# Optimization experiments

Hardware: AMD Instinct MI355X
Metric: run time of the kernel (lower is better)

## Reference

```python
import jax, jax.numpy as jnp
import numpy as np

DIM = 768
NUM_HEADS = 12
HEAD_DIM = DIM // NUM_HEADS
SCALE = HEAD_DIM ** -0.5


def setup_inputs() -> dict:
    key = jax.random.key(0)
    ks = jax.random.split(key, 6)
    B, N, C = 4, 2048, DIM
    x = jax.random.normal(ks[0], (B, N, C), dtype=jnp.float32)
    qkv_weight = jax.random.normal(ks[1], (3 * C, C), dtype=jnp.float32) * (C ** -0.5)
    q_bias = jax.random.normal(ks[2], (C,), dtype=jnp.float32) * 0.02
    v_bias = jax.random.normal(ks[3], (C,), dtype=jnp.float32) * 0.02
    proj_weight = jax.random.normal(ks[4], (C, C), dtype=jnp.float32) * (C ** -0.5)
    proj_bias = jax.random.normal(ks[5], (C,), dtype=jnp.float32) * 0.02
    return {"x": x, "qkv_weight": qkv_weight, "q_bias": q_bias,
            "v_bias": v_bias, "proj_weight": proj_weight, "proj_bias": proj_bias}


def reference(x, qkv_weight, q_bias, v_bias, proj_weight, proj_bias):
    B, N, C = x.shape
    # bias = concat(q_bias, zeros_like(v_bias), v_bias)
    bias = jnp.concatenate([q_bias, jnp.zeros_like(v_bias), v_bias])
    qkv = x @ qkv_weight.T + bias                      # [B, N, 3C]
    qkv = qkv.reshape(B, N, 3, NUM_HEADS, HEAD_DIM)
    q, k, v = jnp.moveaxis(qkv, 2, 0)                  # each [B, N, H, hd]
    q = jnp.transpose(q, (0, 2, 1, 3)) * SCALE         # [B, H, N, hd]
    k = jnp.transpose(k, (0, 2, 1, 3))
    v = jnp.transpose(v, (0, 2, 1, 3))
    attn = jax.nn.softmax(jnp.einsum('bhqd,bhkd->bhqk', q, k), axis=-1)
    out = jnp.einsum('bhqk,bhkd->bhqd', attn, v)       # [B, H, N, hd]
    out = jnp.transpose(out, (0, 2, 1, 3)).reshape(B, N, C)
    return out @ proj_weight.T + proj_bias
```

## Files before the change

kernel.cpp:

```cpp
#include <hip/hip_runtime.h>
#include <cstdint>
#include <cstddef>

typedef _Float16 f16;
typedef _Float16 f16x8 __attribute__((ext_vector_type(8)));
typedef _Float16 f16x4 __attribute__((ext_vector_type(4)));
typedef __fp16 h16x2 __attribute__((ext_vector_type(2)));
typedef float f32x4 __attribute__((ext_vector_type(4)));

#define DIM 768
#define NHEAD 12
#define HD 64
#define BATCH 4
#define SEQ 2048
#define MROWS (BATCH*SEQ)
#define C3 (3*DIM)
#define NBH (BATCH*NHEAD)

__device__ __forceinline__ f32x4 mfma32(f16x8 a, f16x8 b, f32x4 c) {
  return __builtin_amdgcn_mfma_f32_16x16x32_f16(a, b, c, 0, 0, 0);
}
__device__ __forceinline__ f32x4 mfma16(f16x4 a, f16x4 b, f32x4 c) {
  return __builtin_amdgcn_mfma_f32_16x16x16f16(a, b, c, 0, 0, 0);
}

__device__ __forceinline__ void gl2lds16(const void* g, void* l) {
  __builtin_amdgcn_global_load_lds(
      (const __attribute__((address_space(1))) void*)g,
      (__attribute__((address_space(3))) void*)l, 16, 0, 0);
}

__global__ __launch_bounds__(256) void k_convert(
    const float* __restrict__ x, const float* __restrict__ wqkv,
    const float* __restrict__ wproj,
    f16* __restrict__ xh, f16* __restrict__ wqh, f16* __restrict__ wph)
{
  const int NX = MROWS*DIM/4, NW = C3*DIM/4;
  int i = blockIdx.x * 256 + threadIdx.x;
  const float4* src; f16* dst; int idx;
  if (i < NX)         { src = (const float4*)x;     dst = xh;  idx = i; }
  else if (i < NX+NW) { src = (const float4*)wqkv;  dst = wqh; idx = i - NX; }
  else                { src = (const float4*)wproj; dst = wph; idx = i - NX - NW; }
  float4 v = src[idx];
  union { f16 h[4]; uint64_t u; } r;
  r.h[0] = (f16)v.x; r.h[1] = (f16)v.y; r.h[2] = (f16)v.z; r.h[3] = (f16)v.w;
  ((uint64_t*)dst)[idx] = r.u;
}

__device__ __forceinline__ void gemm_tile(
    const f16* __restrict__ A, const f16* __restrict__ B,
    int lda, int ldb, int K, int m0, int n0,
    f16* sA, f16* sB, f32x4 acc[4][4])
{
  const int tid = threadIdx.x, wid = tid >> 6;
  const int lane = tid & 63, lane15 = lane & 15, quad = lane >> 4;
  const int wm = wid >> 1, wn = wid & 1;
  for (int k0 = 0; k0 < K; k0 += 64) {
    __syncthreads();
    #pragma unroll
    for (int i = 0; i < 4; i++) {
      int j = i*256 + tid;
      int row = j >> 3;
      int sc  = (j & 7) ^ (row & 7);
      gl2lds16(A + (size_t)(m0 + row)*lda + k0 + sc*8, sA + (i*256 + wid*64)*8);
      gl2lds16(B + (size_t)(n0 + row)*ldb + k0 + sc*8, sB + (i*256 + wid*64)*8);
    }
    __syncthreads();
    #pragma unroll
    for (int ks = 0; ks < 2; ks++) {
      f16x8 af[4], bf[4];
      #pragma unroll
      for (int t = 0; t < 4; t++) {
        int ra = wm*64 + t*16 + lane15;
        af[t] = *(const f16x8*)(sA + ra*64 + (((ks*4 + quad) ^ (ra & 7)) << 3));
        int rb = wn*64 + t*16 + lane15;
        bf[t] = *(const f16x8*)(sB + rb*64 + (((ks*4 + quad) ^ (rb & 7)) << 3));
      }
      #pragma unroll
      for (int mt = 0; mt < 4; mt++)
        #pragma unroll
        for (int nt = 0; nt < 4; nt++)
          acc[mt][nt] = mfma32(af[mt], bf[nt], acc[mt][nt]);
    }
  }
}

__global__ __launch_bounds__(256, 2) void k_qkv(
    const f16* __restrict__ xh, const f16* __restrict__ wqh,
    const float* __restrict__ q_bias, const float* __restrict__ v_bias,
    f16* __restrict__ Qh, f16* __restrict__ Kh, f16* __restrict__ Vt)
{
  __shared__ f16 sA[128*64], sB[128*64];
  __shared__ f16 sT[128*136];
  f32x4 acc[4][4];
  const f32x4 z4 = {0.f, 0.f, 0.f, 0.f};
  #pragma unroll
  for (int a = 0; a < 4; a++)
    #pragma unroll
    for (int b = 0; b < 4; b++) acc[a][b] = z4;

  const int m0 = blockIdx.y * 128, n0 = blockIdx.x * 128;
  gemm_tile(xh, wqh, DIM, DIM, DIM, m0, n0, sA, sB, acc);

  const int tid = threadIdx.x, wid = tid >> 6, lane = tid & 63;
  const int lane15 = lane & 15, quad = lane >> 4;
  const int wm = wid >> 1, wn = wid & 1;
  const int bb = m0 >> 11, nbase = m0 & (SEQ - 1);
  const float QS = 0.125f * 1.4426950408889634f;

  if (n0 < 2*DIM) {
    const bool isQ = (n0 < DIM);
    #pragma unroll
    for (int nt = 0; nt < 4; nt++) {
      int col_l = wn*64 + nt*16 + lane15;
      int col = n0 + col_l;
      float b = isQ ? q_bias[col] : 0.f;
      #pragma unroll
      for (int mt = 0; mt < 4; mt++)
        #pragma unroll
        for (int r = 0; r < 4; r++) {
          int m_l = wm*64 + mt*16 + quad*4 + r;
          float v = acc[mt][nt][r] + b;
          if (isQ) v *= QS;
          sT[m_l*136 + col_l] = (f16)v;
        }
    }
    __syncthreads();
    #pragma unroll
    for (int it = 0; it < 8; it++) {
      int idx = it*256 + tid;
      int m_l = idx >> 4, ch = idx & 15;
      f16x8 val = *(const f16x8*)(sT + m_l*136 + ch*8);
      int col = n0 + ch*8;
      int c2 = isQ ? col : (col - DIM);
      int h = c2 >> 6, d = c2 & 63;
      f16* dst = isQ ? Qh : Kh;
      *(f16x8*)(dst + (((size_t)(bb*NHEAD + h)*SEQ + nbase + m_l) << 6) + d) = val;
    }
  } else {
    #pragma unroll
    for (int nt = 0; nt < 4; nt++) {
      int col_l = wn*64 + nt*16 + lane15;
      int c2 = n0 - 2*DIM + col_l;
      float b = v_bias[c2];
      #pragma unroll
      for (int mt = 0; mt < 4; mt++)
        #pragma unroll
        for (int r = 0; r < 4; r++) {
          int m_l = wm*64 + mt*16 + quad*4 + r;
          sT[col_l*136 + m_l] = (f16)(acc[mt][nt][r] + b);
        }
    }
    __syncthreads();
    #pragma unroll
    for (int it = 0; it < 8; it++) {
      int idx = it*256 + tid;
      int d_l = idx >> 4, m8 = idx & 15;
      f16x8 val = *(const f16x8*)(sT + d_l*136 + m8*8);
      int c2 = n0 - 2*DIM + d_l;
      int h = c2 >> 6, d = c2 & 63;
      *(f16x8*)(Vt + ((size_t)(bb*NHEAD + h)*HD + d)*SEQ + nbase + m8*8) = val;
    }
  }
}

#define KVT 128
__global__ __launch_bounds__(256, 3) void k_attn(
    const f16* __restrict__ Qh, const f16* __restrict__ Kh,
    const f16* __restrict__ Vt, f16* __restrict__ attnh)
{
  __shared__ f16 smem[4*32*72];
  f16* sV = smem;

  const int tid = threadIdx.x, wid = tid >> 6, lane = tid & 63;
  const int lane15 = lane & 15, quad = lane >> 4;
  const int q0 = blockIdx.x * 128;
  const int bh = blockIdx.y;
  const int qw = q0 + wid*32;

  f16x8 qf[2][2];
  #pragma unroll
  for (int qt = 0; qt < 2; qt++)
    #pragma unroll
    for (int ks = 0; ks < 2; ks++)
      qf[qt][ks] = *(const f16x8*)(Qh + ((size_t)bh*SEQ + qw + qt*16 + lane15)*HD
                                      + ks*32 + quad*8);

  f32x4 o[4][2];
  f32x4 sacc[2];
  const f32x4 z4 = {0.f, 0.f, 0.f, 0.f};
  #pragma unroll
  for (int dt = 0; dt < 4; dt++)
    #pragma unroll
    for (int qt = 0; qt < 2; qt++) o[dt][qt] = z4;
  sacc[0] = z4; sacc[1] = z4;
  const f16x4 one4 = {(f16)1.f, (f16)1.f, (f16)1.f, (f16)1.f};

  const f16* Kbh = Kh + (size_t)bh*SEQ*HD;

  for (int kv0 = 0; kv0 < SEQ; kv0 += KVT) {
    __syncthreads();
    #pragma unroll
    for (int i = 0; i < 4; i++) {
      int j = i*256 + tid;
      int row = j >> 4;
      int sc  = (j & 15) ^ (row & 7);
      gl2lds16(Vt + ((size_t)bh*HD + row)*SEQ + kv0 + sc*8, sV + (i*256 + wid*64)*8);
    }
    __syncthreads();
    const f16* Kt = Kbh + (size_t)kv0*HD;

    #pragma unroll
    for (int c = 0; c < 4; c++) {
      f16x8 ka[2][2];
      #pragma unroll
      for (int kt = 0; kt < 2; kt++)
        #pragma unroll
        for (int ks = 0; ks < 2; ks++)
          ka[ks][kt] = *(const f16x8*)(Kt + (size_t)(c*32 + kt*16 + lane15)*HD
                                          + ks*32 + quad*8);
      f32x4 s[2][2];
      #pragma unroll
      for (int kt = 0; kt < 2; kt++)
        #pragma unroll
        for (int qt = 0; qt < 2; qt++) s[kt][qt] = z4;
      #pragma unroll
      for (int ks = 0; ks < 2; ks++)
        #pragma unroll
        for (int kt = 0; kt < 2; kt++)
          #pragma unroll
          for (int qt = 0; qt < 2; qt++)
            s[kt][qt] = mfma32(ka[ks][kt], qf[qt][ks], s[kt][qt]);

      f16x4 pb[2][2];
      #pragma unroll
      for (int kt = 0; kt < 2; kt++)
        #pragma unroll
        for (int qt = 0; qt < 2; qt++) {
          union { h16x2 g2[2]; f16x4 h4; } u;
          u.g2[0] = __builtin_amdgcn_cvt_pkrtz(exp2f(s[kt][qt][0]), exp2f(s[kt][qt][1]));
          u.g2[1] = __builtin_amdgcn_cvt_pkrtz(exp2f(s[kt][qt][2]), exp2f(s[kt][qt][3]));
          pb[kt][qt] = u.h4;
        }
      #pragma unroll
      for (int kt = 0; kt < 2; kt++)
        #pragma unroll
        for (int qt = 0; qt < 2; qt++)
          sacc[qt] = mfma16(one4, pb[kt][qt], sacc[qt]);

      #pragma unroll
      for (int dt = 0; dt < 4; dt++) {
        int row = dt*16 + lane15;
        #pragma unroll
        for (int kt = 0; kt < 2; kt++) {
          int c16 = 4*c + 2*kt + (quad >> 1);
          const f16* vp = sV + row*KVT + (((c16 ^ (row & 7)) << 3)) + (quad & 1)*4;
          f16x4 va = *(const f16x4*)vp;
          #pragma unroll
          for (int qt = 0; qt < 2; qt++)
            o[dt][qt] = mfma16(va, pb[kt][qt], o[dt][qt]);
        }
      }
    }
  }

  float inv[2] = {1.f / sacc[0][0], 1.f / sacc[1][0]};

  __syncthreads();
  f16* tb = smem + wid * (32 * 72);
  #pragma unroll
  for (int dt = 0; dt < 4; dt++)
    #pragma unroll
    for (int qt = 0; qt < 2; qt++) {
      f32x4 v = o[dt][qt];
      float iv = inv[qt];
      f16x4 hx = {(f16)(v[0]*iv), (f16)(v[1]*iv), (f16)(v[2]*iv), (f16)(v[3]*iv)};
      *(f16x4*)(tb + (qt*16 + lane15)*72 + dt*16 + quad*4) = hx;
    }
  const int b = bh / NHEAD, h = bh % NHEAD;
  #pragma unroll
  for (int i = 0; i < 4; i++) {
    int row = i*8 + (lane >> 3);
    f16x8 rv = *(const f16x8*)(tb + row*72 + (lane & 7)*8);
    *(f16x8*)(attnh + ((size_t)b*SEQ + qw + row)*DIM + h*HD + (lane & 7)*8) = rv;
  }
}

__global__ __launch_bounds__(256, 2) void k_proj(
    const f16* __restrict__ ah, const f16* __restrict__ wph,
    const float* __restrict__ pbias, float* __restrict__ out)
{
  __shared__ f16 sA[128*64], sB[128*64];
  f32x4 acc[4][4];
  const f32x4 z4 = {0.f, 0.f, 0.f, 0.f};
  #pragma unroll
  for (int a = 0; a < 4; a++)
    #pragma unroll
    for (int b = 0; b < 4; b++) acc[a][b] = z4;

  const int m0 = blockIdx.y * 128, n0 = blockIdx.x * 128;
  gemm_tile(ah, wph, DIM, DIM, DIM, m0, n0, sA, sB, acc);

  const int tid = threadIdx.x, wid = tid >> 6, lane = tid & 63;
  const int lane15 = lane & 15, quad = lane >> 4;
  const int wm = wid >> 1, wn = wid & 1;
  #pragma unroll
  for (int nt = 0; nt < 4; nt++) {
    int col = n0 + wn*64 + nt*16 + lane15;
    float bias = pbias[col];
    #pragma unroll
    for (int mt = 0; mt < 4; mt++) {
      #pragma unroll
      for (int r = 0; r < 4; r++) {
        int m = m0 + wm*64 + mt*16 + quad*4 + r;
        out[(size_t)m*DIM + col] = acc[mt][nt][r] + bias;
      }
    }
  }
}

extern "C" void kernel_launch(void* const* d_in, const int* in_sizes, int n_in,
                              void* d_out, int out_size, void* d_ws, size_t ws_size,
                              hipStream_t stream) {
  const float* x    = (const float*)d_in[0];
  const float* wqkv = (const float*)d_in[1];
  const float* qb   = (const float*)d_in[2];
  const float* vb   = (const float*)d_in[3];
  const float* wp   = (const float*)d_in[4];
  const float* pb   = (const float*)d_in[5];
  float* out = (float*)d_out;

  f16* p = (f16*)d_ws;
  f16* xh  = p; p += (size_t)MROWS*DIM;
  f16* wqh = p; p += (size_t)C3*DIM;
  f16* wph = p; p += (size_t)DIM*DIM;
  f16* Qh  = p; p += (size_t)NBH*SEQ*HD;
  f16* Kh  = p; p += (size_t)NBH*SEQ*HD;
  f16* Vt  = p; p += (size_t)NBH*SEQ*HD;
  f16* attnh = xh;

  k_convert<<<8448, 256, 0, stream>>>(x, wqkv, wp, xh, wqh, wph);
  k_qkv<<<dim3(C3/128, MROWS/128), 256, 0, stream>>>(xh, wqh, qb, vb, Qh, Kh, Vt);
  k_attn<<<dim3(SEQ/128, NBH), 256, 0, stream>>>(Qh, Kh, Vt, attnh);
  k_proj<<<dim3(DIM/128, MROWS/128), 256, 0, stream>>>(attnh, wph, pb, out);
}
```

Measured before the change: 254.9 us.

## Double-buffer GEMM tiles and stage K/V through LDS with prefetch in attention

```diff
diff --git a/kernel.cpp b/kernel.cpp
--- a/kernel.cpp
+++ b/kernel.cpp
@@ -50,13 +50,15 @@
 __device__ __forceinline__ void gemm_tile(
     const f16* __restrict__ A, const f16* __restrict__ B,
     int lda, int ldb, int K, int m0, int n0,
-    f16* sA, f16* sB, f32x4 acc[4][4])
-{
+    f16* smem, f32x4 acc[4][4])
+{
+  f16* sA0 = smem;          f16* sA1 = smem + 8192;
+  f16* sB0 = smem + 16384;  f16* sB1 = smem + 24576;
   const int tid = threadIdx.x, wid = tid >> 6;
   const int lane = tid & 63, lane15 = lane & 15, quad = lane >> 4;
   const int wm = wid >> 1, wn = wid & 1;
-  for (int k0 = 0; k0 < K; k0 += 64) {
-    __syncthreads();
+
+  auto stage = [&](int k0, f16* sA, f16* sB) {
     #pragma unroll
     for (int i = 0; i < 4; i++) {
       int j = i*256 + tid;
@@ -65,16 +67,25 @@
       gl2lds16(A + (size_t)(m0 + row)*lda + k0 + sc*8, sA + (i*256 + wid*64)*8);
       gl2lds16(B + (size_t)(n0 + row)*ldb + k0 + sc*8, sB + (i*256 + wid*64)*8);
     }
-    __syncthreads();
+  };
+
+  const int NK = K >> 6;
+  stage(0, sA0, sB0);
+  for (int kk = 0; kk < NK; kk++) {
+    f16* cA = (kk & 1) ? sA1 : sA0;
+    f16* cB = (kk & 1) ? sB1 : sB0;
+    __syncthreads();
+    if (kk + 1 < NK)
+      stage((kk + 1) << 6, (kk & 1) ? sA0 : sA1, (kk & 1) ? sB0 : sB1);
     #pragma unroll
     for (int ks = 0; ks < 2; ks++) {
       f16x8 af[4], bf[4];
       #pragma unroll
       for (int t = 0; t < 4; t++) {
         int ra = wm*64 + t*16 + lane15;
-        af[t] = *(const f16x8*)(sA + ra*64 + (((ks*4 + quad) ^ (ra & 7)) << 3));
+        af[t] = *(const f16x8*)(cA + ra*64 + (((ks*4 + quad) ^ (ra & 7)) << 3));
         int rb = wn*64 + t*16 + lane15;
-        bf[t] = *(const f16x8*)(sB + rb*64 + (((ks*4 + quad) ^ (rb & 7)) << 3));
+        bf[t] = *(const f16x8*)(cB + rb*64 + (((ks*4 + quad) ^ (rb & 7)) << 3));
       }
       #pragma unroll
       for (int mt = 0; mt < 4; mt++)
@@ -90,8 +101,7 @@
     const float* __restrict__ q_bias, const float* __restrict__ v_bias,
     f16* __restrict__ Qh, f16* __restrict__ Kh, f16* __restrict__ Vt)
 {
-  __shared__ f16 sA[128*64], sB[128*64];
-  __shared__ f16 sT[128*136];
+  __shared__ f16 smem[32768];
   f32x4 acc[4][4];
   const f32x4 z4 = {0.f, 0.f, 0.f, 0.f};
   #pragma unroll
@@ -100,13 +110,16 @@
     for (int b = 0; b < 4; b++) acc[a][b] = z4;
 
   const int m0 = blockIdx.y * 128, n0 = blockIdx.x * 128;
-  gemm_tile(xh, wqh, DIM, DIM, DIM, m0, n0, sA, sB, acc);
+  gemm_tile(xh, wqh, DIM, DIM, DIM, m0, n0, smem, acc);
 
   const int tid = threadIdx.x, wid = tid >> 6, lane = tid & 63;
   const int lane15 = lane & 15, quad = lane >> 4;
   const int wm = wid >> 1, wn = wid & 1;
   const int bb = m0 >> 11, nbase = m0 & (SEQ - 1);
   const float QS = 0.125f * 1.4426950408889634f;
+
+  f16* sT = smem;
+  __syncthreads();
 
   if (n0 < 2*DIM) {
     const bool isQ = (n0 < DIM);
@@ -165,12 +178,15 @@
 }
 
 #define KVT 128
+#define NIT (SEQ/KVT)
 __global__ __launch_bounds__(256, 3) void k_attn(
     const f16* __restrict__ Qh, const f16* __restrict__ Kh,
     const f16* __restrict__ Vt, f16* __restrict__ attnh)
 {
-  __shared__ f16 smem[4*32*72];
-  f16* sV = smem;
+  __shared__ f16 smem[2*8192 + 64*132];
+  f16* sK0 = smem;
+  f16* sK1 = smem + 8192;
+  f16* sV  = smem + 16384;
 
   const int tid = threadIdx.x, wid = tid >> 6, lane = tid & 63;
   const int lane15 = lane & 15, quad = lane >> 4;
@@ -178,6 +194,9 @@
   const int bh = blockIdx.y;
   const int qw = q0 + wid*32;
 
+  const f16* Kbh = Kh + (size_t)bh*SEQ*HD;
+  const f16* Vbh = Vt + (size_t)bh*HD*SEQ;
+
   f16x8 qf[2][2];
   #pragma unroll
   for (int qt = 0; qt < 2; qt++)
@@ -196,29 +215,51 @@
   sacc[0] = z4; sacc[1] = z4;
   const f16x4 one4 = {(f16)1.f, (f16)1.f, (f16)1.f, (f16)1.f};
 
-  const f16* Kbh = Kh + (size_t)bh*SEQ*HD;
-
-  for (int kv0 = 0; kv0 < SEQ; kv0 += KVT) {
-    __syncthreads();
+  const int vrow = tid >> 2, vcg = (tid & 3) * 32;
+  const f16* vsrc = Vbh + (size_t)vrow*SEQ + vcg;
+
+  auto stageK = [&](int kv0, f16* sK) {
     #pragma unroll
     for (int i = 0; i < 4; i++) {
       int j = i*256 + tid;
-      int row = j >> 4;
-      int sc  = (j & 15) ^ (row & 7);
-      gl2lds16(Vt + ((size_t)bh*HD + row)*SEQ + kv0 + sc*8, sV + (i*256 + wid*64)*8);
-    }
-    __syncthreads();
-    const f16* Kt = Kbh + (size_t)kv0*HD;
+      int row = j >> 3;
+      int sc  = (j & 7) ^ (row & 7);
+      gl2lds16(Kbh + (size_t)(kv0 + row)*HD + sc*8, sK + (i*256 + wid*64)*8);
+    }
+  };
+
+  stageK(0, sK0);
+  f16x8 vreg[4];
+  #pragma unroll
+  for (int j = 0; j < 4; j++) vreg[j] = *(const f16x8*)(vsrc + j*8);
+
+  for (int it = 0; it < NIT; it++) {
+    f16* cK = (it & 1) ? sK1 : sK0;
+    __syncthreads();
+    #pragma unroll
+    for (int j = 0; j < 4; j++) {
+      union { f16x8 v; f16x4 h[2]; } u; u.v = vreg[j];
+      *(f16x4*)(sV + vrow*132 + vcg + j*8)     = u.h[0];
+      *(f16x4*)(sV + vrow*132 + vcg + j*8 + 4) = u.h[1];
+    }
+    __syncthreads();
+    if (it + 1 < NIT) {
+      stageK((it + 1)*KVT, (it & 1) ? sK0 : sK1);
+      #pragma unroll
+      for (int j = 0; j < 4; j++)
+        vreg[j] = *(const f16x8*)(vsrc + (it + 1)*KVT + j*8);
+    }
 
     #pragma unroll
     for (int c = 0; c < 4; c++) {
       f16x8 ka[2][2];
       #pragma unroll
-      for (int kt = 0; kt < 2; kt++)
+      for (int kt = 0; kt < 2; kt++) {
+        int rb = c*32 + kt*16 + lane15;
         #pragma unroll
         for (int ks = 0; ks < 2; ks++)
-          ka[ks][kt] = *(const f16x8*)(Kt + (size_t)(c*32 + kt*16 + lane15)*HD
-                                          + ks*32 + quad*8);
+          ka[ks][kt] = *(const f16x8*)(cK + rb*64 + (((ks*4 + quad) ^ (rb & 7)) << 3));
+      }
       f32x4 s[2][2];
       #pragma unroll
       for (int kt = 0; kt < 2; kt++)
@@ -254,8 +295,7 @@
         #pragma unroll
         for (int kt = 0; kt < 2; kt++) {
           int c16 = 4*c + 2*kt + (quad >> 1);
-          const f16* vp = sV + row*KVT + (((c16 ^ (row & 7)) << 3)) + (quad & 1)*4;
-          f16x4 va = *(const f16x4*)vp;
+          f16x4 va = *(const f16x4*)(sV + row*132 + c16*8 + (quad & 1)*4);
           #pragma unroll
           for (int qt = 0; qt < 2; qt++)
             o[dt][qt] = mfma16(va, pb[kt][qt], o[dt][qt]);
@@ -277,6 +317,7 @@
       f16x4 hx = {(f16)(v[0]*iv), (f16)(v[1]*iv), (f16)(v[2]*iv), (f16)(v[3]*iv)};
       *(f16x4*)(tb + (qt*16 + lane15)*72 + dt*16 + quad*4) = hx;
     }
+  __syncthreads();
   const int b = bh / NHEAD, h = bh % NHEAD;
   #pragma unroll
   for (int i = 0; i < 4; i++) {
@@ -290,7 +331,7 @@
     const f16* __restrict__ ah, const f16* __restrict__ wph,
     const float* __restrict__ pbias, float* __restrict__ out)
 {
-  __shared__ f16 sA[128*64], sB[128*64];
+  __shared__ f16 smem[32768];
   f32x4 acc[4][4];
   const f32x4 z4 = {0.f, 0.f, 0.f, 0.f};
   #pragma unroll
@@ -299,7 +340,7 @@
     for (int b = 0; b < 4; b++) acc[a][b] = z4;
 
   const int m0 = blockIdx.y * 128, n0 = blockIdx.x * 128;
-  gemm_tile(ah, wph, DIM, DIM, DIM, m0, n0, sA, sB, acc);
+  gemm_tile(ah, wph, DIM, DIM, DIM, m0, n0, smem, acc);
 
   const int tid = threadIdx.x, wid = tid >> 6, lane = tid & 63;
   const int lane15 = lane & 15, quad = lane >> 4;
```

Result: faster. 236.4 us (-7.2%).
